# Performance work log

Hardware: AMD Instinct MI355X
Metric: run time of the kernel (lower is better)

Reference implementation:

```python
import jax, jax.numpy as jnp
import numpy as np

E = 512      # embed_dim
H = 8        # num_heads
HD = E // H  # head_dim
TGT = 512
SRC = 2048
B = 16


def setup_inputs() -> dict:
    key = jax.random.key(0)
    ks = jax.random.split(key, 10)
    inp = {
        "query": jax.random.normal(ks[0], (TGT, B, E), dtype=jnp.float32),
        "key": jax.random.normal(ks[1], (SRC, B, E), dtype=jnp.float32),
        "value": jax.random.normal(ks[2], (SRC, B, E), dtype=jnp.float32),
        "in_proj_weight": jax.random.normal(ks[3], (3 * E, E), dtype=jnp.float32) * 0.02,
        "in_proj_bias": jax.random.normal(ks[4], (3 * E,), dtype=jnp.float32) * 0.02,
        "bias_k": jax.random.normal(ks[5], (1, 1, E), dtype=jnp.float32) * 0.02,
        "bias_v": jax.random.normal(ks[6], (1, 1, E), dtype=jnp.float32) * 0.02,
        "out_proj_weight": jax.random.normal(ks[7], (E, E), dtype=jnp.float32) * 0.02,
        "out_proj_bias": jnp.zeros((E,), dtype=jnp.float32),
        "key_padding_mask": jax.random.randint(ks[8], (B, SRC), 0, 2).astype(bool),
    }
    return inp


def reference(query, key, value, in_proj_weight, in_proj_bias, bias_k, bias_v,
              out_proj_weight, out_proj_bias, key_padding_mask):
    tgt_len, bsz, embed_dim = query.shape
    scaling = float(HD) ** -0.5

    # manual in-projection (query != key, key is value -> separate q, fused kv)
    q = query @ in_proj_weight[:E].T + in_proj_bias[:E]
    k = key @ in_proj_weight[E:2 * E].T + in_proj_bias[E:2 * E]
    v = value @ in_proj_weight[2 * E:].T + in_proj_bias[2 * E:]
    q = q * scaling

    # bias_k / bias_v concatenation along src dim; pad key_padding_mask with False
    k = jnp.concatenate([k, jnp.broadcast_to(bias_k, (1, bsz, E))], axis=0)
    v = jnp.concatenate([v, jnp.broadcast_to(bias_v, (1, bsz, E))], axis=0)
    kpm = jnp.pad(key_padding_mask, ((0, 0), (0, 1)))  # [B, SRC+1]

    src_len = k.shape[0]
    # [len, B, E] -> [B*H, len, HD]
    q = q.reshape(tgt_len, bsz * H, HD).transpose(1, 0, 2)
    k = k.reshape(src_len, bsz * H, HD).transpose(1, 0, 2)
    v = v.reshape(src_len, bsz * H, HD).transpose(1, 0, 2)

    scores = jnp.einsum('bth,bsh->bts', q, k)  # [B*H, TGT, SRC+1]
    mask = kpm[:, None, None, :]               # [B, 1, 1, SRC+1]
    scores = scores.reshape(bsz, H, tgt_len, src_len)
    scores = jnp.where(mask, -jnp.inf, scores).reshape(bsz * H, tgt_len, src_len)
    attn = jax.nn.softmax(scores, axis=-1)

    out = jnp.einsum('bts,bsh->bth', attn, v)                 # [B*H, TGT, HD]
    out = out.transpose(1, 0, 2).reshape(tgt_len, bsz, E)     # [TGT, B, E]
    out = out @ out_proj_weight.T + out_proj_bias
    return out, attn
```

## Files before the change

kernel.cpp:

```cpp
#include <hip/hip_runtime.h>

#define E    512
#define H    8
#define HD   64
#define TGT  512
#define SRC  2048
#define S1   2049
#define S1P  2112
#define NB   16
#define BH   128
#define NCH  33
#define PW   2120

typedef __attribute__((ext_vector_type(8))) short short8;
typedef __attribute__((ext_vector_type(4))) float floatx4;

__device__ __forceinline__ unsigned short f2bf(float x) {
    unsigned u = __float_as_uint(x);
    u = (u + 0x7FFF + ((u >> 16) & 1)) >> 16;
    return (unsigned short)u;
}

__global__ __launch_bounds__(256) void cvt_bf16(const float* __restrict__ src,
    unsigned short* __restrict__ dst, const int n8)
{
    const int i = blockIdx.x * 256 + threadIdx.x;
    if (i >= n8) return;
    const float4 f0 = ((const float4*)src)[(size_t)i * 2];
    const float4 f1 = ((const float4*)src)[(size_t)i * 2 + 1];
    unsigned short o[8] = {f2bf(f0.x), f2bf(f0.y), f2bf(f0.z), f2bf(f0.w),
                           f2bf(f1.x), f2bf(f1.y), f2bf(f1.z), f2bf(f1.w)};
    ((int4*)dst)[i] = *(int4*)o;
}

__global__ __launch_bounds__(256) void proj_gemm(const unsigned short* __restrict__ X,
    const unsigned short* __restrict__ W, const float* __restrict__ bias,
    unsigned short* __restrict__ Y, const int ld, const float scale)
{
    __shared__ __align__(16) unsigned short As[128][72];
    __shared__ __align__(16) unsigned short Bs[64][72];
    const int tid  = threadIdx.x;
    const int c0   = blockIdx.x << 6;
    const int r0   = blockIdx.y << 7;
    const int w    = tid >> 6, lane = tid & 63, c = lane & 15, quad = lane >> 4;
    floatx4 acc[2][4] = {};
    for (int k0 = 0; k0 < E; k0 += 64) {
#pragma unroll
        for (int i = 0; i < 4; ++i) {
            const int idx = tid + (i << 8);
            const int r = idx >> 3, q = (idx & 7) << 3;
            *(int4*)&As[r][q] = *(const int4*)&X[(size_t)(r0 + r) * E + k0 + q];
        }
#pragma unroll
        for (int i = 0; i < 2; ++i) {
            const int idx = tid + (i << 8);
            const int r = idx >> 3, q = (idx & 7) << 3;
            *(int4*)&Bs[r][q] = *(const int4*)&W[(size_t)(c0 + r) * E + k0 + q];
        }
        __syncthreads();
#pragma unroll
        for (int kh = 0; kh < 2; ++kh) {
            short8 a0 = *(const short8*)&As[(w << 5) + c][(kh << 5) + (quad << 3)];
            short8 a1 = *(const short8*)&As[(w << 5) + 16 + c][(kh << 5) + (quad << 3)];
#pragma unroll
            for (int n = 0; n < 4; ++n) {
                short8 b = *(const short8*)&Bs[(n << 4) + c][(kh << 5) + (quad << 3)];
                acc[0][n] = __builtin_amdgcn_mfma_f32_16x16x32_bf16(a0, b, acc[0][n], 0, 0, 0);
                acc[1][n] = __builtin_amdgcn_mfma_f32_16x16x32_bf16(a1, b, acc[1][n], 0, 0, 0);
            }
        }
        __syncthreads();
    }
#pragma unroll
    for (int mt = 0; mt < 2; ++mt) {
#pragma unroll
        for (int reg = 0; reg < 4; ++reg) {
            const int rg = r0 + (w << 5) + (mt << 4) + (quad << 2) + reg;
            const int t = rg >> 4, b = rg & 15;
#pragma unroll
            for (int n = 0; n < 4; ++n) {
                const int col = c0 + (n << 4) + c;
                const int h = col >> 6, hd = col & 63;
                const float v = (acc[mt][n][reg] + bias[col]) * scale;
                Y[((size_t)(b * H + h) * ld + t) * HD + hd] = f2bf(v);
            }
        }
    }
}

#define FB_BIAS  8192
#define FB_KPAD  64512
#define FB_VPAD  516096
__global__ __launch_bounds__(256) void fill_bias(const float* __restrict__ bk,
    const float* __restrict__ bv,
    unsigned short* __restrict__ kbuf, unsigned short* __restrict__ vtbuf)
{
    const int idx = blockIdx.x * 256 + threadIdx.x;
    if (idx < FB_BIAS) {
        const int bh = idx >> 6, hd = idx & 63, h = bh & 7;
        kbuf[((size_t)bh * S1P + SRC) * HD + hd] = f2bf(bk[h * HD + hd]);
        vtbuf[((size_t)bh * HD + hd) * S1P + SRC] = f2bf(bv[h * HD + hd]);
    } else if (idx < FB_BIAS + FB_KPAD) {
        const int i = idx - FB_BIAS;
        const int bh = i / 504, o = i % 504;
        const int4 z = {0, 0, 0, 0};
        ((int4*)&kbuf[((size_t)bh * S1P + S1) * HD])[o] = z;
    } else if (idx < FB_BIAS + FB_KPAD + FB_VPAD) {
        const int i = idx - FB_BIAS - FB_KPAD;
        const int bh = i / 4032, r = i % 4032;
        const int hd = r / 63, s = S1 + r % 63;
        vtbuf[((size_t)bh * HD + hd) * S1P + s] = 0;
    }
}

__global__ __launch_bounds__(256) void transpose_v(const unsigned short* __restrict__ vbuf,
    unsigned short* __restrict__ vtbuf)
{
    __shared__ __align__(16) unsigned short T[64][72];
    const int tid = threadIdx.x;
    const int s0  = blockIdx.x << 6;
    const int bh  = blockIdx.y;
#pragma unroll
    for (int i = 0; i < 2; ++i) {
        const int idx = tid + (i << 8);
        const int s = idx >> 3, q = (idx & 7) << 3;
        *(int4*)&T[s][q] = *(const int4*)&vbuf[((size_t)bh * SRC + s0 + s) * HD + q];
    }
    __syncthreads();
#pragma unroll
    for (int i = 0; i < 2; ++i) {
        const int idx = tid + (i << 8);
        const int hd = idx >> 3, sq = (idx & 7) << 3;
        unsigned short tmp[8];
#pragma unroll
        for (int j = 0; j < 8; ++j) tmp[j] = T[sq + j][hd];
        *(int4*)&vtbuf[((size_t)bh * HD + hd) * S1P + s0 + sq] = *(int4*)tmp;
    }
}

__global__ __launch_bounds__(512, 4) void attn_fused(
    const unsigned short* __restrict__ qbh,
    const unsigned short* __restrict__ kbuf,
    const unsigned short* __restrict__ vtbuf,
    const int* __restrict__ kpm,
    float* __restrict__ attn, unsigned short* __restrict__ ctx)
{
    __shared__ __align__(16) unsigned short P[16][PW];
    __shared__ float cpart[16][68];
    __shared__ float sums[8][16];
    __shared__ float linv[16];
    const int tid = threadIdx.x;
    const int t0  = blockIdx.x << 4;
    const int bh  = blockIdx.y;
    const int bb  = bh >> 3;
    const int w = tid >> 6, lane = tid & 63, c = lane & 15, quad = lane >> 4;

    const unsigned short* qr = &qbh[((size_t)bh * TGT + t0 + c) * HD + (quad << 3)];
    short8 qa0 = *(const short8*)qr;
    short8 qa1 = *(const short8*)(qr + 32);

#define LOADK(D0, D1, M, CH) do {                                               \
        const unsigned short* kb_ = &kbuf[((size_t)bh * S1P + ((CH) << 6)) * HD]; \
        _Pragma("unroll")                                                       \
        for (int n_ = 0; n_ < 4; ++n_) {                                        \
            const unsigned short* kr_ = kb_ + ((n_ << 4) + c) * HD + (quad << 3); \
            D0[n_] = *(const short8*)kr_;                                       \
            D1[n_] = *(const short8*)(kr_ + 32);                                \
        }                                                                       \
        _Pragma("unroll")                                                       \
        for (int n_ = 0; n_ < 4; ++n_) {                                        \
            const int s_ = ((CH) << 6) + (n_ << 4) + c;                         \
            M[n_] = (s_ < SRC) ? (kpm[bb * SRC + s_] ? 3e38f : 0.f)             \
                               : ((s_ == SRC) ? 0.f : 3e38f);                   \
        }                                                                       \
    } while (0)

#define QK_COMPUTE(CH, B0, B1, M) do {                                          \
        const int s0_ = (CH) << 6;                                              \
        floatx4 sc_[4] = {};                                                    \
        _Pragma("unroll")                                                       \
        for (int n_ = 0; n_ < 4; ++n_) {                                        \
            sc_[n_] = __builtin_amdgcn_mfma_f32_16x16x32_bf16(qa0, B0[n_], sc_[n_], 0, 0, 0); \
            sc_[n_] = __builtin_amdgcn_mfma_f32_16x16x32_bf16(qa1, B1[n_], sc_[n_], 0, 0, 0); \
        }                                                                       \
        _Pragma("unroll")                                                       \
        for (int n_ = 0; n_ < 4; ++n_) {                                        \
            _Pragma("unroll")                                                   \
            for (int rg_ = 0; rg_ < 4; ++rg_) {                                 \
                const float p_ = __expf(sc_[n_][rg_] - M[n_]);                  \
                rs[rg_] += p_;                                                  \
                P[(quad << 2) + rg_][s0_ + (n_ << 4) + c] = f2bf(p_);           \
            }                                                                   \
        }                                                                       \
    } while (0)

    float rs[4] = {0.f, 0.f, 0.f, 0.f};
    short8 kb0[4], kb1[4];
    float mk[4];
    LOADK(kb0, kb1, mk, w);
    int ch;
    for (ch = w; ch + 8 < NCH; ch += 8) {
        short8 nb0[4], nb1[4];
        float nm[4];
        LOADK(nb0, nb1, nm, ch + 8);
        QK_COMPUTE(ch, kb0, kb1, mk);
#pragma unroll
        for (int n = 0; n < 4; ++n) { kb0[n] = nb0[n]; kb1[n] = nb1[n]; mk[n] = nm[n]; }
    }
    QK_COMPUTE(ch, kb0, kb1, mk);

#pragma unroll
    for (int reg = 0; reg < 4; ++reg) {
        float v = rs[reg];
        v += __shfl_xor(v, 1); v += __shfl_xor(v, 2);
        v += __shfl_xor(v, 4); v += __shfl_xor(v, 8);
        rs[reg] = v;
    }
    if (c == 0) {
#pragma unroll
        for (int reg = 0; reg < 4; ++reg)
            sums[w][(quad << 2) + reg] = rs[reg];
    }
    __syncthreads();
    if (tid < 16) {
        float s = 0.f;
#pragma unroll
        for (int i = 0; i < 8; ++i) s += sums[i][tid];
        linv[tid] = 1.0f / s;
    }
    __syncthreads();

    const int hs = w & 3, kh2 = w >> 2;
    const int base = kh2 * 1056;
    const unsigned short* vrow = &vtbuf[((size_t)bh * HD + (hs << 4) + c) * S1P + base];
    const unsigned short* prow = &P[c][base];
    floatx4 ca0 = {}, ca1 = {};
#pragma unroll 4
    for (int kc = 0; kc < 16; ++kc) {
        short8 a0 = *(const short8*)&prow[(kc << 6) + (quad << 3)];
        short8 a1 = *(const short8*)&prow[(kc << 6) + 32 + (quad << 3)];
        short8 b0 = *(const short8*)&vrow[(kc << 6) + (quad << 3)];
        short8 b1 = *(const short8*)&vrow[(kc << 6) + 32 + (quad << 3)];
        ca0 = __builtin_amdgcn_mfma_f32_16x16x32_bf16(a0, b0, ca0, 0, 0, 0);
        ca1 = __builtin_amdgcn_mfma_f32_16x16x32_bf16(a1, b1, ca1, 0, 0, 0);
    }
    {
        short8 a = *(const short8*)&prow[1024 + (quad << 3)];
        short8 b = *(const short8*)&vrow[1024 + (quad << 3)];
        ca0 = __builtin_amdgcn_mfma_f32_16x16x32_bf16(a, b, ca0, 0, 0, 0);
    }
    if (kh2 == 1) {
#pragma unroll
        for (int reg = 0; reg < 4; ++reg)
            cpart[(quad << 2) + reg][(hs << 4) + c] = ca0[reg] + ca1[reg];
    }
    __syncthreads();
    if (kh2 == 0) {
#pragma unroll
        for (int reg = 0; reg < 4; ++reg) {
            const int row = (quad << 2) + reg;
            const float v = (ca0[reg] + ca1[reg] + cpart[row][(hs << 4) + c]) * linv[row];
            ctx[((size_t)bh * TGT + t0 + row) * HD + (hs << 4) + c] = f2bf(v);
        }
    }

    for (int c2 = w; c2 < NCH; c2 += 8) {
        const int s0 = c2 << 6;
        if (c2 < 32) {
#pragma unroll
            for (int r = 0; r < 16; ++r) {
                const float p =
                    __uint_as_float((unsigned)P[r][s0 + lane] << 16) * linv[r];
                attn[((size_t)bh * TGT + t0 + r) * S1 + s0 + lane] = p;
            }
        } else if (lane < 16) {
            const float p =
                __uint_as_float((unsigned)P[lane][2048] << 16) * linv[lane];
            attn[((size_t)bh * TGT + t0 + lane) * S1 + 2048] = p;
        }
    }
#undef LOADK
#undef QK_COMPUTE
}

__global__ __launch_bounds__(256) void outproj_gemm(const unsigned short* __restrict__ ctx,
    const unsigned short* __restrict__ W, const float* __restrict__ bias,
    float* __restrict__ out)
{
    __shared__ __align__(16) unsigned short As[128][72];
    __shared__ __align__(16) unsigned short Bs[64][72];
    const int tid = threadIdx.x;
    const int c0  = blockIdx.x << 6;
    const int r0  = blockIdx.y << 7;
    const int w   = tid >> 6, lane = tid & 63, c = lane & 15, quad = lane >> 4;
    floatx4 acc[2][4] = {};
    for (int k0 = 0; k0 < E; k0 += 64) {
        const int h = k0 >> 6;
#pragma unroll
        for (int i = 0; i < 4; ++i) {
            const int idx = tid + (i << 8);
            const int r = idx >> 3, q = (idx & 7) << 3;
            const int rg = r0 + r, t = rg >> 4, b = rg & 15;
            *(int4*)&As[r][q] = *(const int4*)&ctx[((size_t)(b * H + h) * TGT + t) * HD + q];
        }
#pragma unroll
        for (int i = 0; i < 2; ++i) {
            const int idx = tid + (i << 8);
            const int r = idx >> 3, q = (idx & 7) << 3;
            *(int4*)&Bs[r][q] = *(const int4*)&W[(size_t)(c0 + r) * E + k0 + q];
        }
        __syncthreads();
#pragma unroll
        for (int kh = 0; kh < 2; ++kh) {
            short8 a0 = *(const short8*)&As[(w << 5) + c][(kh << 5) + (quad << 3)];
            short8 a1 = *(const short8*)&As[(w << 5) + 16 + c][(kh << 5) + (quad << 3)];
#pragma unroll
            for (int n = 0; n < 4; ++n) {
                short8 b = *(const short8*)&Bs[(n << 4) + c][(kh << 5) + (quad << 3)];
                acc[0][n] = __builtin_amdgcn_mfma_f32_16x16x32_bf16(a0, b, acc[0][n], 0, 0, 0);
                acc[1][n] = __builtin_amdgcn_mfma_f32_16x16x32_bf16(a1, b, acc[1][n], 0, 0, 0);
            }
        }
        __syncthreads();
    }
#pragma unroll
    for (int mt = 0; mt < 2; ++mt) {
#pragma unroll
        for (int reg = 0; reg < 4; ++reg) {
            const int rg = r0 + (w << 5) + (mt << 4) + (quad << 2) + reg;
#pragma unroll
            for (int n = 0; n < 4; ++n) {
                const int col = c0 + (n << 4) + c;
                out[(size_t)rg * E + col] = acc[mt][n][reg] + bias[col];
            }
        }
    }
}

extern "C" void kernel_launch(void* const* d_in, const int* in_sizes, int n_in,
                              void* d_out, int out_size, void* d_ws, size_t ws_size,
                              hipStream_t stream)
{
    const float* query  = (const float*)d_in[0];
    const float* key    = (const float*)d_in[1];
    const float* value  = (const float*)d_in[2];
    const float* ipw    = (const float*)d_in[3];
    const float* ipb    = (const float*)d_in[4];
    const float* bias_k = (const float*)d_in[5];
    const float* bias_v = (const float*)d_in[6];
    const float* opw    = (const float*)d_in[7];
    const float* opb    = (const float*)d_in[8];
    const int*   kpm    = (const int*)d_in[9];

    float* out  = (float*)d_out;
    float* attn = out + (size_t)TGT * NB * E;

    unsigned short* k_bf = (unsigned short*)attn;
    unsigned short* v_bf = k_bf + (size_t)16777216;
    unsigned short* vbuf = v_bf + (size_t)16777216;

    char* ws = (char*)d_ws;
    unsigned short* q_bf  = (unsigned short*)ws;
    unsigned short* wi_bf = q_bf  + (size_t)4194304;
    unsigned short* wo_bf = wi_bf + (size_t)786432;
    unsigned short* qbh   = wo_bf + (size_t)262144;
    unsigned short* kbuf  = qbh   + (size_t)4194304;
    unsigned short* vtbuf = kbuf  + (size_t)17301504;
    unsigned short* ctx   = vtbuf + (size_t)17301504;

    cvt_bf16<<<dim3(2048), 256, 0, stream>>>(query, q_bf, 524288);
    cvt_bf16<<<dim3(8192), 256, 0, stream>>>(key,   k_bf, 2097152);
    cvt_bf16<<<dim3(8192), 256, 0, stream>>>(value, v_bf, 2097152);
    cvt_bf16<<<dim3(384),  256, 0, stream>>>(ipw,   wi_bf, 98304);
    cvt_bf16<<<dim3(128),  256, 0, stream>>>(opw,   wo_bf, 32768);

    proj_gemm<<<dim3(8, 64),  256, 0, stream>>>(q_bf, wi_bf,          ipb,         qbh,  TGT, 0.125f);
    proj_gemm<<<dim3(8, 256), 256, 0, stream>>>(k_bf, wi_bf + 262144, ipb + E,     kbuf, S1P, 1.0f);
    proj_gemm<<<dim3(8, 256), 256, 0, stream>>>(v_bf, wi_bf + 524288, ipb + 2 * E, vbuf, SRC, 1.0f);

    fill_bias<<<dim3(2300), 256, 0, stream>>>(bias_k, bias_v, kbuf, vtbuf);
    transpose_v<<<dim3(32, 128), 256, 0, stream>>>(vbuf, vtbuf);

    attn_fused<<<dim3(32, 128), 512, 0, stream>>>(qbh, kbuf, vtbuf, kpm, attn, ctx);
    outproj_gemm<<<dim3(8, 64), 256, 0, stream>>>(ctx, wo_bf, opb, out);
}
```

Before: 1.083 ms.

## Fuse bf16 conversion into GEMM loads, swizzle attention blocks, restructure attention loops

Drops the separate fp32-to-bf16 conversion kernels. The projection and output GEMMs now read fp32 directly and convert while staging tiles into shared memory, which saves a full write and re-read of the converted key/value tensors. The attention kernel also remaps block indices with a swizzle to change how blocks are placed, fully unrolls the QK chunk loop with double-buffered K loads, software-pipelines the V loads in the PV loop, and writes the attention matrix two columns per lane. In exchange, the GEMMs read twice the bytes per tile and repeat the weight conversion in every block.

New measurement: 1.161 ms. 7.2% more time.

```diff
diff --git a/kernel.cpp b/kernel.cpp
--- a/kernel.cpp
+++ b/kernel.cpp
@@ -21,20 +21,8 @@
     return (unsigned short)u;
 }
 
-__global__ __launch_bounds__(256) void cvt_bf16(const float* __restrict__ src,
-    unsigned short* __restrict__ dst, const int n8)
-{
-    const int i = blockIdx.x * 256 + threadIdx.x;
-    if (i >= n8) return;
-    const float4 f0 = ((const float4*)src)[(size_t)i * 2];
-    const float4 f1 = ((const float4*)src)[(size_t)i * 2 + 1];
-    unsigned short o[8] = {f2bf(f0.x), f2bf(f0.y), f2bf(f0.z), f2bf(f0.w),
-                           f2bf(f1.x), f2bf(f1.y), f2bf(f1.z), f2bf(f1.w)};
-    ((int4*)dst)[i] = *(int4*)o;
-}
-
-__global__ __launch_bounds__(256) void proj_gemm(const unsigned short* __restrict__ X,
-    const unsigned short* __restrict__ W, const float* __restrict__ bias,
+__global__ __launch_bounds__(256) void proj_gemm(const float* __restrict__ X,
+    const float* __restrict__ W, const float* __restrict__ bias,
     unsigned short* __restrict__ Y, const int ld, const float scale)
 {
     __shared__ __align__(16) unsigned short As[128][72];
@@ -49,13 +37,21 @@
         for (int i = 0; i < 4; ++i) {
             const int idx = tid + (i << 8);
             const int r = idx >> 3, q = (idx & 7) << 3;
-            *(int4*)&As[r][q] = *(const int4*)&X[(size_t)(r0 + r) * E + k0 + q];
+            const float4 f0 = *(const float4*)&X[(size_t)(r0 + r) * E + k0 + q];
+            const float4 f1 = *(const float4*)&X[(size_t)(r0 + r) * E + k0 + q + 4];
+            unsigned short o[8] = {f2bf(f0.x), f2bf(f0.y), f2bf(f0.z), f2bf(f0.w),
+                                   f2bf(f1.x), f2bf(f1.y), f2bf(f1.z), f2bf(f1.w)};
+            *(int4*)&As[r][q] = *(int4*)o;
         }
 #pragma unroll
         for (int i = 0; i < 2; ++i) {
             const int idx = tid + (i << 8);
             const int r = idx >> 3, q = (idx & 7) << 3;
-            *(int4*)&Bs[r][q] = *(const int4*)&W[(size_t)(c0 + r) * E + k0 + q];
+            const float4 f0 = *(const float4*)&W[(size_t)(c0 + r) * E + k0 + q];
+            const float4 f1 = *(const float4*)&W[(size_t)(c0 + r) * E + k0 + q + 4];
+            unsigned short o[8] = {f2bf(f0.x), f2bf(f0.y), f2bf(f0.z), f2bf(f0.w),
+                                   f2bf(f1.x), f2bf(f1.y), f2bf(f1.z), f2bf(f1.w)};
+            *(int4*)&Bs[r][q] = *(int4*)o;
         }
         __syncthreads();
 #pragma unroll
@@ -149,10 +145,12 @@
     __shared__ float cpart[16][68];
     __shared__ float sums[8][16];
     __shared__ float linv[16];
-    const int tid = threadIdx.x;
-    const int t0  = blockIdx.x << 4;
-    const int bh  = blockIdx.y;
-    const int bb  = bh >> 3;
+    const int tid  = threadIdx.x;
+    const int orig = blockIdx.y * 32 + blockIdx.x;
+    const int swz  = (orig & 7) * 512 + (orig >> 3);
+    const int t0   = (swz & 31) << 4;
+    const int bh   = swz >> 5;
+    const int bb   = bh >> 3;
     const int w = tid >> 6, lane = tid & 63, c = lane & 15, quad = lane >> 4;
 
     const unsigned short* qr = &qbh[((size_t)bh * TGT + t0 + c) * HD + (quad << 3)];
@@ -195,19 +193,16 @@
     } while (0)
 
     float rs[4] = {0.f, 0.f, 0.f, 0.f};
-    short8 kb0[4], kb1[4];
-    float mk[4];
-    LOADK(kb0, kb1, mk, w);
-    int ch;
-    for (ch = w; ch + 8 < NCH; ch += 8) {
-        short8 nb0[4], nb1[4];
-        float nm[4];
-        LOADK(nb0, nb1, nm, ch + 8);
-        QK_COMPUTE(ch, kb0, kb1, mk);
-#pragma unroll
-        for (int n = 0; n < 4; ++n) { kb0[n] = nb0[n]; kb1[n] = nb1[n]; mk[n] = nm[n]; }
-    }
-    QK_COMPUTE(ch, kb0, kb1, mk);
+    short8 ka0[4], ka1[4], kb0[4], kb1[4];
+    float ma[4], mb[4];
+    LOADK(ka0, ka1, ma, w);
+    LOADK(kb0, kb1, mb, w + 8);
+    QK_COMPUTE(w,      ka0, ka1, ma);  LOADK(ka0, ka1, ma, w + 16);
+    QK_COMPUTE(w + 8,  kb0, kb1, mb);  LOADK(kb0, kb1, mb, w + 24);
+    QK_COMPUTE(w + 16, ka0, ka1, ma);
+    if (w == 0) LOADK(ka0, ka1, ma, 32);
+    QK_COMPUTE(w + 24, kb0, kb1, mb);
+    if (w == 0) QK_COMPUTE(32, ka0, ka1, ma);
 
 #pragma unroll
     for (int reg = 0; reg < 4; ++reg) {
@@ -233,22 +228,21 @@
     const int hs = w & 3, kh2 = w >> 2;
     const int base = kh2 * 1056;
     const unsigned short* vrow = &vtbuf[((size_t)bh * HD + (hs << 4) + c) * S1P + base];
-    const unsigned short* prow = &P[c][base];
+#define LV(U) (*(const short8*)&vrow[((U) << 5) + (quad << 3)])
+#define LP(U) (*(const short8*)&P[c][base + ((U) << 5) + (quad << 3)])
     floatx4 ca0 = {}, ca1 = {};
-#pragma unroll 4
-    for (int kc = 0; kc < 16; ++kc) {
-        short8 a0 = *(const short8*)&prow[(kc << 6) + (quad << 3)];
-        short8 a1 = *(const short8*)&prow[(kc << 6) + 32 + (quad << 3)];
-        short8 b0 = *(const short8*)&vrow[(kc << 6) + (quad << 3)];
-        short8 b1 = *(const short8*)&vrow[(kc << 6) + 32 + (quad << 3)];
-        ca0 = __builtin_amdgcn_mfma_f32_16x16x32_bf16(a0, b0, ca0, 0, 0, 0);
-        ca1 = __builtin_amdgcn_mfma_f32_16x16x32_bf16(a1, b1, ca1, 0, 0, 0);
-    }
-    {
-        short8 a = *(const short8*)&prow[1024 + (quad << 3)];
-        short8 b = *(const short8*)&vrow[1024 + (quad << 3)];
-        ca0 = __builtin_amdgcn_mfma_f32_16x16x32_bf16(a, b, ca0, 0, 0, 0);
-    }
+    short8 vt = LV(32);
+    short8 v0 = LV(0), v1 = LV(1), v2 = LV(2), v3 = LV(3);
+#pragma unroll
+    for (int u = 0; u < 32; u += 4) {
+        ca0 = __builtin_amdgcn_mfma_f32_16x16x32_bf16(LP(u),     v0, ca0, 0, 0, 0);
+        ca1 = __builtin_amdgcn_mfma_f32_16x16x32_bf16(LP(u + 1), v1, ca1, 0, 0, 0);
+        if (u < 28) { v0 = LV(u + 4); v1 = LV(u + 5); }
+        ca0 = __builtin_amdgcn_mfma_f32_16x16x32_bf16(LP(u + 2), v2, ca0, 0, 0, 0);
+        ca1 = __builtin_amdgcn_mfma_f32_16x16x32_bf16(LP(u + 3), v3, ca1, 0, 0, 0);
+        if (u < 28) { v2 = LV(u + 6); v3 = LV(u + 7); }
+    }
+    ca0 = __builtin_amdgcn_mfma_f32_16x16x32_bf16(LP(32), vt, ca0, 0, 0, 0);
     if (kh2 == 1) {
 #pragma unroll
         for (int reg = 0; reg < 4; ++reg)
@@ -264,27 +258,29 @@
         }
     }
 
-    for (int c2 = w; c2 < NCH; c2 += 8) {
-        const int s0 = c2 << 6;
-        if (c2 < 32) {
-#pragma unroll
-            for (int r = 0; r < 16; ++r) {
-                const float p =
-                    __uint_as_float((unsigned)P[r][s0 + lane] << 16) * linv[r];
-                attn[((size_t)bh * TGT + t0 + r) * S1 + s0 + lane] = p;
-            }
-        } else if (lane < 16) {
-            const float p =
-                __uint_as_float((unsigned)P[lane][2048] << 16) * linv[lane];
-            attn[((size_t)bh * TGT + t0 + lane) * S1 + 2048] = p;
-        }
+    for (int p = w; p < 16; p += 8) {
+        const int s0 = p << 7;
+#pragma unroll
+        for (int r = 0; r < 16; ++r) {
+            const unsigned pk = *(const unsigned*)&P[r][s0 + (lane << 1)];
+            const float li = linv[r];
+            const size_t a = ((size_t)bh * TGT + t0 + r) * S1 + s0 + (lane << 1);
+            attn[a]     = __uint_as_float((pk & 0xFFFFu) << 16) * li;
+            attn[a + 1] = __uint_as_float(pk & 0xFFFF0000u) * li;
+        }
+    }
+    if (w == 7 && lane < 16) {
+        const float p = __uint_as_float((unsigned)P[lane][2048] << 16) * linv[lane];
+        attn[((size_t)bh * TGT + t0 + lane) * S1 + 2048] = p;
     }
 #undef LOADK
 #undef QK_COMPUTE
+#undef LV
+#undef LP
 }
 
 __global__ __launch_bounds__(256) void outproj_gemm(const unsigned short* __restrict__ ctx,
-    const unsigned short* __restrict__ W, const float* __restrict__ bias,
+    const float* __restrict__ W, const float* __restrict__ bias,
     float* __restrict__ out)
 {
     __shared__ __align__(16) unsigned short As[128][72];
@@ -307,7 +303,11 @@
         for (int i = 0; i < 2; ++i) {
             const int idx = tid + (i << 8);
             const int r = idx >> 3, q = (idx & 7) << 3;
-            *(int4*)&Bs[r][q] = *(const int4*)&W[(size_t)(c0 + r) * E + k0 + q];
+            const float4 f0 = *(const float4*)&W[(size_t)(c0 + r) * E + k0 + q];
+            const float4 f1 = *(const float4*)&W[(size_t)(c0 + r) * E + k0 + q + 4];
+            unsigned short o[8] = {f2bf(f0.x), f2bf(f0.y), f2bf(f0.z), f2bf(f0.w),
+                                   f2bf(f1.x), f2bf(f1.y), f2bf(f1.z), f2bf(f1.w)};
+            *(int4*)&Bs[r][q] = *(int4*)o;
         }
         __syncthreads();
 #pragma unroll
@@ -355,32 +355,21 @@
     float* out  = (float*)d_out;
     float* attn = out + (size_t)TGT * NB * E;
 
-    unsigned short* k_bf = (unsigned short*)attn;
-    unsigned short* v_bf = k_bf + (size_t)16777216;
-    unsigned short* vbuf = v_bf + (size_t)16777216;
+    unsigned short* vbuf = (unsigned short*)attn;
 
     char* ws = (char*)d_ws;
-    unsigned short* q_bf  = (unsigned short*)ws;
-    unsigned short* wi_bf = q_bf  + (size_t)4194304;
-    unsigned short* wo_bf = wi_bf + (size_t)786432;
-    unsigned short* qbh   = wo_bf + (size_t)262144;
+    unsigned short* qbh   = (unsigned short*)ws;
     unsigned short* kbuf  = qbh   + (size_t)4194304;
     unsigned short* vtbuf = kbuf  + (size_t)17301504;
     unsigned short* ctx   = vtbuf + (size_t)17301504;
 
-    cvt_bf16<<<dim3(2048), 256, 0, stream>>>(query, q_bf, 524288);
-    cvt_bf16<<<dim3(8192), 256, 0, stream>>>(key,   k_bf, 2097152);
-    cvt_bf16<<<dim3(8192), 256, 0, stream>>>(value, v_bf, 2097152);
-    cvt_bf16<<<dim3(384),  256, 0, stream>>>(ipw,   wi_bf, 98304);
-    cvt_bf16<<<dim3(128),  256, 0, stream>>>(opw,   wo_bf, 32768);
-
-    proj_gemm<<<dim3(8, 64),  256, 0, stream>>>(q_bf, wi_bf,          ipb,         qbh,  TGT, 0.125f);
-    proj_gemm<<<dim3(8, 256), 256, 0, stream>>>(k_bf, wi_bf + 262144, ipb + E,     kbuf, S1P, 1.0f);
-    proj_gemm<<<dim3(8, 256), 256, 0, stream>>>(v_bf, wi_bf + 524288, ipb + 2 * E, vbuf, SRC, 1.0f);
+    proj_gemm<<<dim3(8, 64),  256, 0, stream>>>(query, ipw,           ipb,         qbh,  TGT, 0.125f);
+    proj_gemm<<<dim3(8, 256), 256, 0, stream>>>(key,   ipw + 262144,  ipb + E,     kbuf, S1P, 1.0f);
+    proj_gemm<<<dim3(8, 256), 256, 0, stream>>>(value, ipw + 524288,  ipb + 2 * E, vbuf, SRC, 1.0f);
 
     fill_bias<<<dim3(2300), 256, 0, stream>>>(bias_k, bias_v, kbuf, vtbuf);
     transpose_v<<<dim3(32, 128), 256, 0, stream>>>(vbuf, vtbuf);
 
     attn_fused<<<dim3(32, 128), 512, 0, stream>>>(qbh, kbuf, vtbuf, kpm, attn, ctx);
-    outproj_gemm<<<dim3(8, 64), 256, 0, stream>>>(ctx, wo_bf, opb, out);
-}
+    outproj_gemm<<<dim3(8, 64), 256, 0, stream>>>(ctx, opw, opb, out);
+}
```

## Use hardware bf16 conversion, pin K prefetch registers, software-pipeline PV loads, widen attn writeback

Applied to the files above, without the earlier changes.

Replaces the manual round-to-nearest bf16 conversion with the HIP bf16 intrinsics, including packed pair conversion in the input cast kernel. An empty asm statement pins the prefetched K fragments in registers so the compiler cannot sink the loads past the QK compute. The P·V loop is fully unrolled with V fragments loaded a step ahead of the MFMAs. The attention-probability writeback now reads two bf16 values per lane from shared memory over 128-wide chunks, with the bias column handled separately. Together these target conversion ALU cost, load latency and shared-memory read count, at the cost of more register pressure and stores that are no longer contiguous 4-byte per lane.

Result: no change. 1.075 ms (-0.7%).

```diff
diff --git a/kernel.cpp b/kernel.cpp
--- a/kernel.cpp
+++ b/kernel.cpp
@@ -1,4 +1,5 @@
 #include <hip/hip_runtime.h>
+#include <hip/hip_bf16.h>
 
 #define E    512
 #define H    8
@@ -21,6 +22,20 @@
     return (unsigned short)u;
 }
 
+__device__ __forceinline__ unsigned short f2bf1(float x) {
+    __hip_bfloat16 h = __float2bfloat16(x);
+    return *(unsigned short*)&h;
+}
+
+__device__ __forceinline__ int4 cvt8(const float4 f0, const float4 f1) {
+    __hip_bfloat162 o[4];
+    o[0] = __float22bfloat162_rn({f0.x, f0.y});
+    o[1] = __float22bfloat162_rn({f0.z, f0.w});
+    o[2] = __float22bfloat162_rn({f1.x, f1.y});
+    o[3] = __float22bfloat162_rn({f1.z, f1.w});
+    return *(int4*)o;
+}
+
 __global__ __launch_bounds__(256) void cvt_bf16(const float* __restrict__ src,
     unsigned short* __restrict__ dst, const int n8)
 {
@@ -28,9 +43,7 @@
     if (i >= n8) return;
     const float4 f0 = ((const float4*)src)[(size_t)i * 2];
     const float4 f1 = ((const float4*)src)[(size_t)i * 2 + 1];
-    unsigned short o[8] = {f2bf(f0.x), f2bf(f0.y), f2bf(f0.z), f2bf(f0.w),
-                           f2bf(f1.x), f2bf(f1.y), f2bf(f1.z), f2bf(f1.w)};
-    ((int4*)dst)[i] = *(int4*)o;
+    ((int4*)dst)[i] = cvt8(f0, f1);
 }
 
 __global__ __launch_bounds__(256) void proj_gemm(const unsigned short* __restrict__ X,
@@ -82,7 +95,7 @@
                 const int col = c0 + (n << 4) + c;
                 const int h = col >> 6, hd = col & 63;
                 const float v = (acc[mt][n][reg] + bias[col]) * scale;
-                Y[((size_t)(b * H + h) * ld + t) * HD + hd] = f2bf(v);
+                Y[((size_t)(b * H + h) * ld + t) * HD + hd] = f2bf1(v);
             }
         }
     }
@@ -175,6 +188,10 @@
         }                                                                       \
     } while (0)
 
+#define PIN(D0, D1) asm volatile("" :                                          \
+        "+v"(D0[0]), "+v"(D0[1]), "+v"(D0[2]), "+v"(D0[3]),                     \
+        "+v"(D1[0]), "+v"(D1[1]), "+v"(D1[2]), "+v"(D1[3]))
+
 #define QK_COMPUTE(CH, B0, B1, M) do {                                          \
         const int s0_ = (CH) << 6;                                              \
         floatx4 sc_[4] = {};                                                    \
@@ -189,7 +206,7 @@
             for (int rg_ = 0; rg_ < 4; ++rg_) {                                 \
                 const float p_ = __expf(sc_[n_][rg_] - M[n_]);                  \
                 rs[rg_] += p_;                                                  \
-                P[(quad << 2) + rg_][s0_ + (n_ << 4) + c] = f2bf(p_);           \
+                P[(quad << 2) + rg_][s0_ + (n_ << 4) + c] = f2bf1(p_);          \
             }                                                                   \
         }                                                                       \
     } while (0)
@@ -203,6 +220,7 @@
         short8 nb0[4], nb1[4];
         float nm[4];
         LOADK(nb0, nb1, nm, ch + 8);
+        PIN(nb0, nb1);
         QK_COMPUTE(ch, kb0, kb1, mk);
 #pragma unroll
         for (int n = 0; n < 4; ++n) { kb0[n] = nb0[n]; kb1[n] = nb1[n]; mk[n] = nm[n]; }
@@ -233,22 +251,21 @@
     const int hs = w & 3, kh2 = w >> 2;
     const int base = kh2 * 1056;
     const unsigned short* vrow = &vtbuf[((size_t)bh * HD + (hs << 4) + c) * S1P + base];
-    const unsigned short* prow = &P[c][base];
+#define LV(U) (*(const short8*)&vrow[((U) << 5) + (quad << 3)])
+#define LP(U) (*(const short8*)&P[c][base + ((U) << 5) + (quad << 3)])
     floatx4 ca0 = {}, ca1 = {};
-#pragma unroll 4
-    for (int kc = 0; kc < 16; ++kc) {
-        short8 a0 = *(const short8*)&prow[(kc << 6) + (quad << 3)];
-        short8 a1 = *(const short8*)&prow[(kc << 6) + 32 + (quad << 3)];
-        short8 b0 = *(const short8*)&vrow[(kc << 6) + (quad << 3)];
-        short8 b1 = *(const short8*)&vrow[(kc << 6) + 32 + (quad << 3)];
-        ca0 = __builtin_amdgcn_mfma_f32_16x16x32_bf16(a0, b0, ca0, 0, 0, 0);
-        ca1 = __builtin_amdgcn_mfma_f32_16x16x32_bf16(a1, b1, ca1, 0, 0, 0);
-    }
-    {
-        short8 a = *(const short8*)&prow[1024 + (quad << 3)];
-        short8 b = *(const short8*)&vrow[1024 + (quad << 3)];
-        ca0 = __builtin_amdgcn_mfma_f32_16x16x32_bf16(a, b, ca0, 0, 0, 0);
-    }
+    short8 vt = LV(32);
+    short8 v0 = LV(0), v1 = LV(1), v2 = LV(2), v3 = LV(3);
+#pragma unroll
+    for (int u = 0; u < 32; u += 4) {
+        ca0 = __builtin_amdgcn_mfma_f32_16x16x32_bf16(LP(u),     v0, ca0, 0, 0, 0);
+        ca1 = __builtin_amdgcn_mfma_f32_16x16x32_bf16(LP(u + 1), v1, ca1, 0, 0, 0);
+        if (u < 28) { v0 = LV(u + 4); v1 = LV(u + 5); }
+        ca0 = __builtin_amdgcn_mfma_f32_16x16x32_bf16(LP(u + 2), v2, ca0, 0, 0, 0);
+        ca1 = __builtin_amdgcn_mfma_f32_16x16x32_bf16(LP(u + 3), v3, ca1, 0, 0, 0);
+        if (u < 28) { v2 = LV(u + 6); v3 = LV(u + 7); }
+    }
+    ca0 = __builtin_amdgcn_mfma_f32_16x16x32_bf16(LP(32), vt, ca0, 0, 0, 0);
     if (kh2 == 1) {
 #pragma unroll
         for (int reg = 0; reg < 4; ++reg)
@@ -260,27 +277,30 @@
         for (int reg = 0; reg < 4; ++reg) {
             const int row = (quad << 2) + reg;
             const float v = (ca0[reg] + ca1[reg] + cpart[row][(hs << 4) + c]) * linv[row];
-            ctx[((size_t)bh * TGT + t0 + row) * HD + (hs << 4) + c] = f2bf(v);
-        }
-    }
-
-    for (int c2 = w; c2 < NCH; c2 += 8) {
-        const int s0 = c2 << 6;
-        if (c2 < 32) {
-#pragma unroll
-            for (int r = 0; r < 16; ++r) {
-                const float p =
-                    __uint_as_float((unsigned)P[r][s0 + lane] << 16) * linv[r];
-                attn[((size_t)bh * TGT + t0 + r) * S1 + s0 + lane] = p;
-            }
-        } else if (lane < 16) {
-            const float p =
-                __uint_as_float((unsigned)P[lane][2048] << 16) * linv[lane];
-            attn[((size_t)bh * TGT + t0 + lane) * S1 + 2048] = p;
-        }
+            ctx[((size_t)bh * TGT + t0 + row) * HD + (hs << 4) + c] = f2bf1(v);
+        }
+    }
+
+    for (int p = w; p < 16; p += 8) {
+        const int s0 = p << 7;
+#pragma unroll
+        for (int r = 0; r < 16; ++r) {
+            const unsigned pk = *(const unsigned*)&P[r][s0 + (lane << 1)];
+            const float li = linv[r];
+            const size_t a = ((size_t)bh * TGT + t0 + r) * S1 + s0 + (lane << 1);
+            attn[a]     = __uint_as_float((pk & 0xFFFFu) << 16) * li;
+            attn[a + 1] = __uint_as_float(pk & 0xFFFF0000u) * li;
+        }
+    }
+    if (w == 7 && lane < 16) {
+        const float p = __uint_as_float((unsigned)P[lane][2048] << 16) * linv[lane];
+        attn[((size_t)bh * TGT + t0 + lane) * S1 + 2048] = p;
     }
 #undef LOADK
+#undef PIN
 #undef QK_COMPUTE
+#undef LV
+#undef LP
 }
 
 __global__ __launch_bounds__(256) void outproj_gemm(const unsigned short* __restrict__ ctx,
```
